# Kernel optimization log

Hardware: AMD Instinct MI355X
Metric: run time of the kernel (lower is better)

Reference implementation:

```python
import jax, jax.numpy as jnp
import numpy as np

B, N_BLOCK, D_MODEL = 4096, 64, 256


def setup_inputs() -> dict:
    key = jax.random.key(0)
    k1, k2 = jax.random.split(key)
    h = jax.random.normal(k1, (B, N_BLOCK, D_MODEL), dtype=jnp.float32)
    # xavier_normal_ for square [d, d]: std = sqrt(2/(d+d)) = 1/sqrt(d)
    W_a = jax.random.normal(k2, (D_MODEL, D_MODEL), dtype=jnp.float32) / jnp.sqrt(
        jnp.float32(D_MODEL))
    b_a = jnp.zeros((N_BLOCK, D_MODEL), dtype=jnp.float32)
    return {"h": h, "W_a": W_a, "b_a": b_a}


def reference(h, W_a, b_a):
    # h: [B, n_block, d_model]
    # scores = tanh(h @ W_a + b_a): [B, n_block, d_model]
    s = jnp.tanh(jnp.einsum("bnd,de->bne", h, W_a) + b_a)
    # Original applies Softmax(dim=1) to a [1, n_block, d_model] chunk,
    # i.e. normalization is over the n_block axis.
    a = jax.nn.softmax(s, axis=1)
    # elementwise weight then full sum per block -> [B, n_block]
    return jnp.sum(a * h, axis=2)
```

## Files before the change

kernel.cpp:

```cpp
#include <hip/hip_runtime.h>

#define BATCH 4096
#define NB    64
#define DM    256
#define PITCH 264

typedef __bf16 bf16x8 __attribute__((ext_vector_type(8)));
typedef float  f32x4  __attribute__((ext_vector_type(4)));

union Frag16 { uint4 u; bf16x8 b; ushort s[8]; };

__device__ __forceinline__ ushort f2bf(float x) {
    unsigned u = __float_as_uint(x);
    unsigned r = (u + 0x7FFFu + ((u >> 16) & 1u)) >> 16;
    return (ushort)r;
}
__device__ __forceinline__ float bf2f(ushort u) {
    return __uint_as_float(((unsigned)u) << 16);
}

__global__ void swizzle_W(const float* __restrict__ W, ushort* __restrict__ Wf) {
    int idx  = blockIdx.x * 256 + threadIdx.x;
    int lane = idx & 63;
    int ks   = (idx >> 6) & 7;
    int et   = idx >> 9;
    int e    = et * 16 + (lane & 15);
    int k0   = ks * 32 + ((lane >> 4) << 3);
    Frag16 f;
#pragma unroll
    for (int j = 0; j < 8; ++j)
        f.s[j] = f2bf(W[(k0 + j) * DM + e]);
    reinterpret_cast<uint4*>(Wf)[idx] = f.u;
}

__global__ __launch_bounds__(256) void aspect_attn(
    const float*  __restrict__ h,
    const ushort* __restrict__ Wf,
    const float*  __restrict__ ba,
    float*        __restrict__ out)
{
    __shared__ __align__(16) ushort Hs[NB * PITCH];
    __shared__ float op[4][NB];

    const int tid  = threadIdx.x;
    const int wave = tid >> 6;
    const int lane = tid & 63;
    const int quad = lane >> 4;
    const int l15  = lane & 15;
    const int b    = blockIdx.x;

    const float* hb = h + (size_t)b * (NB * DM);

#pragma unroll
    for (int it = 0; it < 16; ++it) {
        int g   = it * 256 + tid;
        int row = g >> 6;
        int c   = (g & 63) << 2;
        f32x4 v = reinterpret_cast<const f32x4*>(hb)[g];
        ushort4 o;
        o.x = f2bf(v.x); o.y = f2bf(v.y); o.z = f2bf(v.z); o.w = f2bf(v.w);
        *reinterpret_cast<ushort4*>(&Hs[row * PITCH + c]) = o;
    }
    __syncthreads();

    f32x4 acc[4][4];
#pragma unroll
    for (int mt = 0; mt < 4; ++mt)
#pragma unroll
        for (int nt = 0; nt < 4; ++nt) {
            f32x4 z = {0.f, 0.f, 0.f, 0.f};
            acc[mt][nt] = z;
        }

    const uint4* WfB = reinterpret_cast<const uint4*>(Wf);
#pragma unroll
    for (int ks = 0; ks < 8; ++ks) {
        Frag16 af[4], bfr[4];
#pragma unroll
        for (int mt = 0; mt < 4; ++mt) {
            int row = mt * 16 + l15;
            af[mt].u = *reinterpret_cast<const uint4*>(&Hs[row * PITCH + ks * 32 + quad * 8]);
        }
#pragma unroll
        for (int nt = 0; nt < 4; ++nt)
            bfr[nt].u = WfB[(((wave * 4 + nt) * 8) + ks) * 64 + lane];
#pragma unroll
        for (int mt = 0; mt < 4; ++mt)
#pragma unroll
            for (int nt = 0; nt < 4; ++nt)
                acc[mt][nt] = __builtin_amdgcn_mfma_f32_16x16x32_bf16(
                    af[mt].b, bfr[nt].b, acc[mt][nt], 0, 0, 0);
    }

    const int colbase = wave * 64;

#pragma unroll
    for (int mt = 0; mt < 4; ++mt)
#pragma unroll
        for (int r = 0; r < 4; ++r) {
            int row = mt * 16 + quad * 4 + r;
#pragma unroll
            for (int nt = 0; nt < 4; ++nt) {
                int col = colbase + nt * 16 + l15;
                float x = acc[mt][nt][r] + ba[row * DM + col];
                float e = __expf(-2.f * fabsf(x));
                float t = (1.f - e) * __builtin_amdgcn_rcpf(1.f + e);
                acc[mt][nt][r] = copysignf(t, x);
            }
        }

#pragma unroll
    for (int nt = 0; nt < 4; ++nt) {
        float ls = 0.f;
#pragma unroll
        for (int mt = 0; mt < 4; ++mt)
#pragma unroll
            for (int r = 0; r < 4; ++r) {
                float p = __expf(acc[mt][nt][r]);
                acc[mt][nt][r] = p;
                ls += p;
            }
        ls += __shfl_xor(ls, 16, 64);
        ls += __shfl_xor(ls, 32, 64);
        float inv = __builtin_amdgcn_rcpf(ls);
#pragma unroll
        for (int mt = 0; mt < 4; ++mt)
#pragma unroll
            for (int r = 0; r < 4; ++r)
                acc[mt][nt][r] *= inv;
    }

#pragma unroll
    for (int mt = 0; mt < 4; ++mt)
#pragma unroll
        for (int r = 0; r < 4; ++r) {
            int row = mt * 16 + quad * 4 + r;
            float s = 0.f;
#pragma unroll
            for (int nt = 0; nt < 4; ++nt) {
                int col = colbase + nt * 16 + l15;
                s += acc[mt][nt][r] * bf2f(Hs[row * PITCH + col]);
            }
#pragma unroll
            for (int m = 1; m < 16; m <<= 1)
                s += __shfl_xor(s, m, 64);
            if (l15 == 0) op[wave][row] = s;
        }
    __syncthreads();

    if (tid < NB)
        out[(size_t)b * NB + tid] = op[0][tid] + op[1][tid] + op[2][tid] + op[3][tid];
}

extern "C" void kernel_launch(void* const* d_in, const int* in_sizes, int n_in,
                              void* d_out, int out_size, void* d_ws, size_t ws_size,
                              hipStream_t stream) {
    const float* h  = (const float*)d_in[0];
    const float* W  = (const float*)d_in[1];
    const float* ba = (const float*)d_in[2];
    float* out = (float*)d_out;
    ushort* Wf = (ushort*)d_ws;

    swizzle_W<<<32, 256, 0, stream>>>(W, Wf);
    aspect_attn<<<BATCH, 256, 0, stream>>>(h, Wf, ba, out);
}
```

Before: 415.2 us.

## Fold bias into MFMA via identity fragments and store H in fragment-major LDS layout

Converts the bias to bf16 and appends it to the swizzled weight buffer. It is added through two extra MFMA k-steps whose A fragments are identity rows, which removes the per-element global bias loads in the epilogue. The LDS copy of H is stored directly in MFMA fragment order, so A-fragment reads become contiguous 16-byte loads. Packed bf16 conversion and launch_bounds(256,4) are also added. The cost is extra MFMA work and bias quantised to bf16.

New measurement: 406.8 us. 1.02x faster.

```diff
diff --git a/kernel.cpp b/kernel.cpp
--- a/kernel.cpp
+++ b/kernel.cpp
@@ -1,45 +1,54 @@
 #include <hip/hip_runtime.h>
+#include <hip/hip_bf16.h>
 
 #define BATCH 4096
 #define NB    64
 #define DM    256
-#define PITCH 264
+#define KSW   8
+#define KST   10
 
 typedef __bf16 bf16x8 __attribute__((ext_vector_type(8)));
 typedef float  f32x4  __attribute__((ext_vector_type(4)));
 
 union Frag16 { uint4 u; bf16x8 b; ushort s[8]; };
+union Pk2    { __hip_bfloat162 v; unsigned u; };
 
 __device__ __forceinline__ ushort f2bf(float x) {
     unsigned u = __float_as_uint(x);
-    unsigned r = (u + 0x7FFFu + ((u >> 16) & 1u)) >> 16;
-    return (ushort)r;
+    return (ushort)((u + 0x7FFFu + ((u >> 16) & 1u)) >> 16);
+}
+__device__ __forceinline__ unsigned pk2(float a, float b) {
+    Pk2 p; p.v = __float22bfloat162_rn(make_float2(a, b));
+    return p.u;
 }
 __device__ __forceinline__ float bf2f(ushort u) {
     return __uint_as_float(((unsigned)u) << 16);
 }
 
-__global__ void swizzle_W(const float* __restrict__ W, ushort* __restrict__ Wf) {
+__global__ void swizzle_WB(const float* __restrict__ W, const float* __restrict__ ba,
+                           ushort* __restrict__ Wf) {
     int idx  = blockIdx.x * 256 + threadIdx.x;
     int lane = idx & 63;
-    int ks   = (idx >> 6) & 7;
-    int et   = idx >> 9;
+    int g    = idx >> 6;
+    int et   = g / KST;
+    int ks   = g % KST;
     int e    = et * 16 + (lane & 15);
-    int k0   = ks * 32 + ((lane >> 4) << 3);
+    int r0   = (ks < KSW) ? ks * 32 : (ks - KSW) * 32;
+    r0 += ((lane >> 4) << 3);
+    const float* src = (ks < KSW) ? W : ba;
     Frag16 f;
 #pragma unroll
     for (int j = 0; j < 8; ++j)
-        f.s[j] = f2bf(W[(k0 + j) * DM + e]);
+        f.s[j] = f2bf(src[(r0 + j) * DM + e]);
     reinterpret_cast<uint4*>(Wf)[idx] = f.u;
 }
 
-__global__ __launch_bounds__(256) void aspect_attn(
+__global__ __launch_bounds__(256, 4) void aspect_attn(
     const float*  __restrict__ h,
     const ushort* __restrict__ Wf,
-    const float*  __restrict__ ba,
     float*        __restrict__ out)
 {
-    __shared__ __align__(16) ushort Hs[NB * PITCH];
+    __shared__ __align__(16) ushort Hs[2048 * 8];
     __shared__ float op[4][NB];
 
     const int tid  = threadIdx.x;
@@ -52,14 +61,17 @@
     const float* hb = h + (size_t)b * (NB * DM);
 
 #pragma unroll
-    for (int it = 0; it < 16; ++it) {
-        int g   = it * 256 + tid;
-        int row = g >> 6;
-        int c   = (g & 63) << 2;
-        f32x4 v = reinterpret_cast<const f32x4*>(hb)[g];
-        ushort4 o;
-        o.x = f2bf(v.x); o.y = f2bf(v.y); o.z = f2bf(v.z); o.w = f2bf(v.w);
-        *reinterpret_cast<ushort4*>(&Hs[row * PITCH + c]) = o;
+    for (int it = 0; it < 8; ++it) {
+        int slot = it * 256 + tid;
+        int f    = slot >> 6;
+        int row  = ((f >> 3) << 4) | l15;
+        int k0   = ((f & 7) << 5) | (quad << 3);
+        const f32x4* p = reinterpret_cast<const f32x4*>(hb + row * DM + k0);
+        f32x4 a = p[0], c = p[1];
+        uint4 o;
+        o.x = pk2(a.x, a.y); o.y = pk2(a.z, a.w);
+        o.z = pk2(c.x, c.y); o.w = pk2(c.z, c.w);
+        reinterpret_cast<uint4*>(Hs)[slot] = o;
     }
     __syncthreads();
 
@@ -73,17 +85,38 @@
         }
 
     const uint4* WfB = reinterpret_cast<const uint4*>(Wf);
+    const uint4* HsB = reinterpret_cast<const uint4*>(Hs);
+
 #pragma unroll
-    for (int ks = 0; ks < 8; ++ks) {
+    for (int ks = 0; ks < KSW; ++ks) {
         Frag16 af[4], bfr[4];
 #pragma unroll
-        for (int mt = 0; mt < 4; ++mt) {
-            int row = mt * 16 + l15;
-            af[mt].u = *reinterpret_cast<const uint4*>(&Hs[row * PITCH + ks * 32 + quad * 8]);
-        }
+        for (int mt = 0; mt < 4; ++mt)
+            af[mt].u = HsB[(mt * 8 + ks) * 64 + lane];
 #pragma unroll
         for (int nt = 0; nt < 4; ++nt)
-            bfr[nt].u = WfB[(((wave * 4 + nt) * 8) + ks) * 64 + lane];
+            bfr[nt].u = WfB[((wave * 4 + nt) * KST + ks) * 64 + lane];
+#pragma unroll
+        for (int mt = 0; mt < 4; ++mt)
+#pragma unroll
+            for (int nt = 0; nt < 4; ++nt)
+                acc[mt][nt] = __builtin_amdgcn_mfma_f32_16x16x32_bf16(
+                    af[mt].b, bfr[nt].b, acc[mt][nt], 0, 0, 0);
+    }
+#pragma unroll
+    for (int kx = 0; kx < 2; ++kx) {
+        Frag16 af[4], bfr[4];
+#pragma unroll
+        for (int nt = 0; nt < 4; ++nt)
+            bfr[nt].u = WfB[((wave * 4 + nt) * KST + KSW + kx) * 64 + lane];
+        const int kb = kx * 32 + quad * 8;
+#pragma unroll
+        for (int mt = 0; mt < 4; ++mt) {
+            int d = (mt * 16 + l15) - kb;
+#pragma unroll
+            for (int j = 0; j < 8; ++j)
+                af[mt].s[j] = (d == j) ? (ushort)0x3F80 : (ushort)0;
+        }
 #pragma unroll
         for (int mt = 0; mt < 4; ++mt)
 #pragma unroll
@@ -92,22 +125,17 @@
                     af[mt].b, bfr[nt].b, acc[mt][nt], 0, 0, 0);
     }
 
-    const int colbase = wave * 64;
-
 #pragma unroll
     for (int mt = 0; mt < 4; ++mt)
 #pragma unroll
-        for (int r = 0; r < 4; ++r) {
-            int row = mt * 16 + quad * 4 + r;
+        for (int nt = 0; nt < 4; ++nt)
 #pragma unroll
-            for (int nt = 0; nt < 4; ++nt) {
-                int col = colbase + nt * 16 + l15;
-                float x = acc[mt][nt][r] + ba[row * DM + col];
+            for (int r = 0; r < 4; ++r) {
+                float x = acc[mt][nt][r];
                 float e = __expf(-2.f * fabsf(x));
                 float t = (1.f - e) * __builtin_amdgcn_rcpf(1.f + e);
                 acc[mt][nt][r] = copysignf(t, x);
             }
-        }
 
 #pragma unroll
     for (int nt = 0; nt < 4; ++nt) {
@@ -130,16 +158,19 @@
                 acc[mt][nt][r] *= inv;
     }
 
+    const int colb = wave * 64;
 #pragma unroll
     for (int mt = 0; mt < 4; ++mt)
 #pragma unroll
         for (int r = 0; r < 4; ++r) {
-            int row = mt * 16 + quad * 4 + r;
+            const int row  = mt * 16 + quad * 4 + r;
+            const int ridx = mt * 4096 + (quad * 4 + r) * 8;
             float s = 0.f;
 #pragma unroll
             for (int nt = 0; nt < 4; ++nt) {
-                int col = colbase + nt * 16 + l15;
-                s += acc[mt][nt][r] * bf2f(Hs[row * PITCH + col]);
+                int col  = colb + nt * 16 + l15;
+                int coff = (col >> 5) * 512 + ((col >> 3) & 3) * 128 + (col & 7);
+                s += acc[mt][nt][r] * bf2f(Hs[ridx + coff]);
             }
 #pragma unroll
             for (int m = 1; m < 16; m <<= 1)
@@ -161,6 +192,6 @@
     float* out = (float*)d_out;
     ushort* Wf = (ushort*)d_ws;
 
-    swizzle_W<<<32, 256, 0, stream>>>(W, Wf);
-    aspect_attn<<<BATCH, 256, 0, stream>>>(h, Wf, ba, out);
+    swizzle_WB<<<40, 256, 0, stream>>>(W, ba, Wf);
+    aspect_attn<<<BATCH, 256, 0, stream>>>(h, Wf, out);
 }
```
